# Kernel optimization log

Measured on AMD Instinct MI355X. Metric: run time of the kernel, lower is better.

## Reference

```python
import jax, jax.numpy as jnp
import numpy as np

B = 8192
MOTION_DIM = 512
COMMAND_DIM = 64
HIDDEN = 1024
E = 8  # num_experts
NUM_LAYERS = 6


def _dense(key, shape, fan_in):
    return jax.random.normal(key, shape, dtype=jnp.float32) * (1.0 / np.sqrt(fan_in))


def setup_inputs() -> dict:
    key = jax.random.key(0)
    ks = jax.random.split(key, 32)
    in_dim = MOTION_DIM + COMMAND_DIM  # 576
    inp = {
        "motion": jax.random.normal(ks[0], (B, MOTION_DIM), dtype=jnp.float32),
        "command": jax.random.normal(ks[1], (B, COMMAND_DIM), dtype=jnp.float32),
        # gating network: in -> H -> H -> E, ELU, softmax
        "g_w1": _dense(ks[2], (in_dim, HIDDEN), in_dim),
        "g_b1": jnp.zeros((HIDDEN,), jnp.float32),
        "g_w2": _dense(ks[3], (HIDDEN, HIDDEN), HIDDEN),
        "g_b2": jnp.zeros((HIDDEN,), jnp.float32),
        "g_w3": _dense(ks[4], (HIDDEN, E), HIDDEN),
        "g_b3": jnp.zeros((E,), jnp.float32),
        # MoE layers: dims [in->H, H->H, H->H, H->H, H->H?, ...] per CMG layout
        "w0": _dense(ks[5], (E, in_dim, HIDDEN), in_dim),
        "b0": jnp.zeros((E, HIDDEN), jnp.float32),
        "w1": _dense(ks[6], (E, HIDDEN, HIDDEN), HIDDEN),
        "b1": jnp.zeros((E, HIDDEN), jnp.float32),
        "w2": _dense(ks[7], (E, HIDDEN, HIDDEN), HIDDEN),
        "b2": jnp.zeros((E, HIDDEN), jnp.float32),
        "w3": _dense(ks[8], (E, HIDDEN, HIDDEN), HIDDEN),
        "b3": jnp.zeros((E, HIDDEN), jnp.float32),
        "w4": _dense(ks[9], (E, HIDDEN, HIDDEN), HIDDEN),
        "b4": jnp.zeros((E, HIDDEN), jnp.float32),
        "w5": _dense(ks[10], (E, HIDDEN, MOTION_DIM), HIDDEN),
        "b5": jnp.zeros((E, MOTION_DIM), jnp.float32),
    }
    return inp


def _moe_layer(x, coeffs, W, b):
    # x: [B, din], coeffs: [B, E], W: [E, din, dout], b: [E, dout]
    # y[b] = sum_e coeffs[b,e] * (x[b] @ W[e] + b[e])
    y = jnp.einsum("be,bi,eio->bo", coeffs, x, W)
    y = y + jnp.einsum("be,eo->bo", coeffs, b)
    return y


def _cmg_forward(motion, command,
                 g_w1, g_b1, g_w2, g_b2, g_w3, g_b3,
                 w0, b0, w1, b1, w2, b2, w3, b3, w4, b4, w5, b5):
    x = jnp.concatenate([motion, command], axis=-1)  # [B, in_dim]
    # gating network
    g = jax.nn.elu(x @ g_w1 + g_b1)
    g = jax.nn.elu(g @ g_w2 + g_b2)
    coeffs = jax.nn.softmax(g @ g_w3 + g_b3, axis=-1)  # [B, E]
    # stacked MoE layers with ELU between all but last
    Ws = [w0, w1, w2, w3, w4, w5]
    bs = [b0, b1, b2, b3, b4, b5]
    for i in range(NUM_LAYERS):
        x = _moe_layer(x, coeffs, Ws[i], bs[i])
        if i < NUM_LAYERS - 1:
            x = jax.nn.elu(x)
    return x  # [B, MOTION_DIM]


def reference(motion, command,
              g_w1, g_b1, g_w2, g_b2, g_w3, g_b3,
              w0, b0, w1, b1, w2, b2, w3, b3, w4, b4, w5, b5):
    return _cmg_forward(motion, command,
                        g_w1, g_b1, g_w2, g_b2, g_w3, g_b3,
                        w0, b0, w1, b1, w2, b2, w3, b3, w4, b4, w5, b5)
```

## Files before the change

kernel.cpp:

```cpp
#include <hip/hip_runtime.h>
#include <hip/hip_bf16.h>

typedef __attribute__((ext_vector_type(8))) short bf16x8;
typedef __attribute__((ext_vector_type(4))) float f32x4;

__device__ __forceinline__ float bf2f(unsigned short u) {
    union { unsigned int i; float f; } v; v.i = ((unsigned int)u) << 16; return v.f;
}
__device__ __forceinline__ unsigned short f2bf(float f) {
    union { float f; unsigned int i; } v; v.f = f;
    unsigned int x = v.i;
    return (unsigned short)((x + 0x7FFFu + ((x >> 16) & 1u)) >> 16);
}

__device__ __forceinline__ void gload_lds16(const unsigned short* g, unsigned short* l) {
    __builtin_amdgcn_global_load_lds(
        (const __attribute__((address_space(1))) unsigned int*)g,
        (__attribute__((address_space(3))) unsigned int*)l,
        16, 0, 0);
}

#define VM4  asm volatile("s_waitcnt vmcnt(4)" ::: "memory")
#define VM0  asm volatile("s_waitcnt vmcnt(0)" ::: "memory")
#define LG0  asm volatile("s_waitcnt lgkmcnt(0)" ::: "memory")
#define SB0  __builtin_amdgcn_sched_barrier(0)

__global__ void concat_cvt(const float* __restrict__ motion,
                           const float* __restrict__ command,
                           unsigned short* __restrict__ out) {
    int id = blockIdx.x * 256 + threadIdx.x;
    int b = id / 144, q = id % 144;
    float4 v;
    if (q < 128) v = *(const float4*)(motion + (size_t)b * 512 + q * 4);
    else         v = *(const float4*)(command + (size_t)b * 64 + (q - 128) * 4);
    ushort4 o;
    o.x = f2bf(v.x); o.y = f2bf(v.y); o.z = f2bf(v.z); o.w = f2bf(v.w);
    *(ushort4*)(out + (size_t)b * 576 + q * 4) = o;
}

__global__ void transpose_cvt(const float* __restrict__ in,
                              unsigned short* __restrict__ out,
                              int K, int N, int tpe) {
    __shared__ unsigned short tile[64][72];
    int e = blockIdx.x / tpe, r = blockIdx.x % tpe;
    in  += (size_t)e * K * N;
    out += (size_t)e * N * K;
    int nbn = N / 64;
    int k0 = (r / nbn) * 64;
    int n0 = (r % nbn) * 64;
    int t = threadIdx.x;
    int tx = t & 63, ty = t >> 6;
    #pragma unroll
    for (int rr = 0; rr < 16; ++rr) {
        int kr = ty + rr * 4;
        tile[kr][tx] = f2bf(in[(size_t)(k0 + kr) * N + n0 + tx]);
    }
    __syncthreads();
    int txh = t & 31, tyh = t >> 5;
    #pragma unroll
    for (int rr = 0; rr < 8; ++rr) {
        int nr = tyh + rr * 8;
        unsigned int vlo = tile[2 * txh][nr];
        unsigned int vhi = tile[2 * txh + 1][nr];
        unsigned int* o32 = (unsigned int*)(out + (size_t)(n0 + nr) * K + k0);
        o32[txh] = vlo | (vhi << 16);
    }
}

__global__ __launch_bounds__(256) void gating_kernel(
    const unsigned short* __restrict__ g2,
    const float* __restrict__ w3, const float* __restrict__ b3,
    float* __restrict__ coeffs) {
    __shared__ float w3s[8][1024];
    int t = threadIdx.x;
    for (int i = t; i < 1024; i += 256) {
        #pragma unroll
        for (int e = 0; e < 8; ++e) w3s[e][i] = w3[(size_t)i * 8 + e];
    }
    __syncthreads();
    int lane = t & 63, wv = t >> 6;
    int row = blockIdx.x * 4 + wv;
    const unsigned short* xr = g2 + (size_t)row * 1024;
    float acc[8];
    #pragma unroll
    for (int e = 0; e < 8; ++e) acc[e] = 0.f;
    for (int it = 0; it < 16; ++it) {
        float xv = bf2f(xr[lane + it * 64]);
        #pragma unroll
        for (int e = 0; e < 8; ++e) acc[e] += xv * w3s[e][lane + it * 64];
    }
    #pragma unroll
    for (int e = 0; e < 8; ++e) {
        float v = acc[e];
        #pragma unroll
        for (int off = 32; off; off >>= 1) v += __shfl_xor(v, off);
        acc[e] = v + b3[e];
    }
    float mx = acc[0];
    #pragma unroll
    for (int e = 1; e < 8; ++e) mx = fmaxf(mx, acc[e]);
    float s = 0.f;
    #pragma unroll
    for (int e = 0; e < 8; ++e) { acc[e] = __expf(acc[e] - mx); s += acc[e]; }
    float inv = 1.f / s;
    if (lane < 8) coeffs[(size_t)row * 8 + lane] = acc[lane] * inv;
}

template<bool DO_ELU>
__global__ __launch_bounds__(256, 4)
void gemm_bf16(const unsigned short* __restrict__ A,
               const unsigned short* __restrict__ BT,
               const float* __restrict__ bias,
               unsigned short* __restrict__ Out,
               int N, int ld, int kpart) {
    __shared__ unsigned short As[128 * 64];
    __shared__ unsigned short Bs[128 * 64];
    int ntn = N >> 7;
    int nwg = gridDim.x;
    int bid = blockIdx.x;
    { int cpx = nwg >> 3; bid = (bid & 7) * cpx + (bid >> 3); }
    int tm = bid / ntn, tn = bid - tm * ntn;
    int row0 = tm << 7, col0 = tn << 7;
    int t = threadIdx.x;
    int lane = t & 63;
    int wid = t >> 6;
    int wr = wid >> 1, wc = wid & 1;
    const unsigned short* Ab = A + (size_t)(row0 + wid * 32 + (lane >> 3)) * ld + (lane & 7) * 8;
    const unsigned short* Bb = BT + (size_t)(col0 + wid * 32 + (lane >> 3)) * ld + (lane & 7) * 8;
    unsigned short* Asd = &As[wid * 32 * 64];
    unsigned short* Bsd = &Bs[wid * 32 * 64];
    f32x4 acc[4][4];
    #pragma unroll
    for (int i = 0; i < 4; ++i)
        #pragma unroll
        for (int j = 0; j < 4; ++j) acc[i][j] = (f32x4){0.f, 0.f, 0.f, 0.f};
    int nkt = kpart >> 6;
    for (int kt = 0; kt < nkt; ++kt) {
        size_t ko = (size_t)kt << 6;
        #pragma unroll
        for (int q = 0; q < 4; ++q) {
            gload_lds16(Ab + (size_t)(q * 8) * ld + ko, Asd + q * 8 * 64);
            gload_lds16(Bb + (size_t)(q * 8) * ld + ko, Bsd + q * 8 * 64);
        }
        __syncthreads();
        #pragma unroll
        for (int kk = 0; kk < 2; ++kk) {
            bf16x8 af[4], bfr[4];
            #pragma unroll
            for (int m = 0; m < 4; ++m)
                af[m] = *(const bf16x8*)(&As[(wr * 64 + m * 16 + (lane & 15)) * 64 + kk * 32 + (lane >> 4) * 8]);
            #pragma unroll
            for (int n = 0; n < 4; ++n)
                bfr[n] = *(const bf16x8*)(&Bs[(wc * 64 + n * 16 + (lane & 15)) * 64 + kk * 32 + (lane >> 4) * 8]);
            #pragma unroll
            for (int m = 0; m < 4; ++m)
                #pragma unroll
                for (int n = 0; n < 4; ++n)
                    acc[m][n] = __builtin_amdgcn_mfma_f32_16x16x32_bf16(af[m], bfr[n], acc[m][n], 0, 0, 0);
        }
        __syncthreads();
    }
    #pragma unroll
    for (int m = 0; m < 4; ++m) {
        int rbase = row0 + wr * 64 + m * 16 + ((lane >> 4) << 2);
        #pragma unroll
        for (int n = 0; n < 4; ++n) {
            int cg = col0 + wc * 64 + n * 16 + (lane & 15);
            float bv = bias[cg];
            #pragma unroll
            for (int r2 = 0; r2 < 4; ++r2) {
                float v = acc[m][n][r2] + bv;
                if (DO_ELU) v = v > 0.f ? v : (__expf(v) - 1.f);
                Out[(size_t)(rbase + r2) * N + cg] = f2bf(v);
            }
        }
    }
}

template<bool DO_ELU, bool OUT_F32>
__global__ __launch_bounds__(512, 1)
void gemm_fused(const unsigned short* __restrict__ A,
                const unsigned short* __restrict__ BT,
                const float* __restrict__ coeffs,
                const float* __restrict__ bias,
                void* __restrict__ Out,
                int K, int dout) {
    __shared__ unsigned short lds[65536];

    int ntn = dout >> 5;
    int nwg = gridDim.x;
    int bid = blockIdx.x;
    { int cpx = nwg >> 3; bid = (bid & 7) * cpx + (bid >> 3); }
    int tm = bid / ntn, tn = bid - tm * ntn;
    int row0 = tm << 8;
    int c0 = tn << 5;
    int nkt = K >> 5;

    int t = threadIdx.x;
    int lane = t & 63, wid = t >> 6;
    int wm = wid >> 2, wn = wid & 3;
    int q = lane >> 4;

    int aoff[8], boff[4];
    #pragma unroll
    for (int m = 0; m < 8; ++m) {
        int row = wm * 128 + m * 16 + (lane & 15);
        aoff[m] = row * 32 + ((q ^ ((row >> 1) & 3)) << 3);
    }
    #pragma unroll
    for (int n = 0; n < 4; ++n) {
        int row = wn * 64 + n * 16 + (lane & 15);
        boff[n] = 8192 + row * 32 + ((q ^ ((row >> 1) & 3)) << 3);
    }

    int srow = t >> 2;
    int scol = ((t & 3) ^ ((t >> 3) & 3)) * 8;
    const unsigned short* Asrc = A + (size_t)(row0 + srow) * K + scol;
    int br0 = (srow >> 5) * dout + c0 + (srow & 31);
    int br1 = ((srow + 128) >> 5) * dout + c0 + (srow & 31);
    const unsigned short* Bsrc0 = BT + (size_t)br0 * K + scol;
    const unsigned short* Bsrc1 = BT + (size_t)br1 * K + scol;
    int wdst = wid * 512;

    f32x4 acc[8][4];
    #pragma unroll
    for (int m = 0; m < 8; ++m)
        #pragma unroll
        for (int n = 0; n < 4; ++n) acc[m][n] = (f32x4){0.f, 0.f, 0.f, 0.f};

    #pragma unroll
    for (int S = 0; S < 2; ++S) {
        gload_lds16(Asrc + S * 32,                   &lds[S * 16384 + wdst]);
        gload_lds16(Asrc + (size_t)128 * K + S * 32, &lds[S * 16384 + 4096 + wdst]);
        gload_lds16(Bsrc0 + S * 32,                  &lds[S * 16384 + 8192 + wdst]);
        gload_lds16(Bsrc1 + S * 32,                  &lds[S * 16384 + 12288 + wdst]);
    }
    VM4; SB0;
    __builtin_amdgcn_s_barrier();

    for (int s = 0; s < nkt; ++s) {
        int sb = (s & 3) << 14;
        bool st = (s + 2) < nkt;
        int rb2 = ((s + 2) & 3) << 14;
        int ko2 = (s + 2) * 32;

        if (st) {
            gload_lds16(Asrc + ko2,                   &lds[rb2 + wdst]);
            gload_lds16(Asrc + (size_t)128 * K + ko2, &lds[rb2 + 4096 + wdst]);
            gload_lds16(Bsrc0 + ko2,                  &lds[rb2 + 8192 + wdst]);
            gload_lds16(Bsrc1 + ko2,                  &lds[rb2 + 12288 + wdst]);
        }
        SB0;
        if (s + 1 < nkt) {
            if (st) { VM4; } else { VM0; }
        }
        SB0;
        __builtin_amdgcn_s_barrier();
        SB0;

        bf16x8 bfrg[4], afr[8];
        #pragma unroll
        for (int n = 0; n < 4; ++n)
            bfrg[n] = *(const bf16x8*)(&lds[sb + boff[n]]);
        #pragma unroll
        for (int m = 0; m < 8; ++m)
            afr[m] = *(const bf16x8*)(&lds[sb + aoff[m]]);
        __builtin_amdgcn_s_setprio(1);
        #pragma unroll
        for (int m = 0; m < 8; ++m)
            #pragma unroll
            for (int n = 0; n < 4; ++n)
                acc[m][n] = __builtin_amdgcn_mfma_f32_16x16x32_bf16(bfrg[n], afr[m], acc[m][n], 0, 0, 0);
        __builtin_amdgcn_s_setprio(0);
        SB0;
    }

    float* plds = (float*)lds;
    __syncthreads();
    {
        int e0 = 2 * wn, e1 = e0 + 1;
        f32x4 b0h[2], b1h[2];
        #pragma unroll
        for (int h = 0; h < 2; ++h) {
            float4 u0 = *(const float4*)(bias + e0 * dout + c0 + h * 16 + q * 4);
            float4 u1 = *(const float4*)(bias + e1 * dout + c0 + h * 16 + q * 4);
            b0h[h] = (f32x4){u0.x, u0.y, u0.z, u0.w};
            b1h[h] = (f32x4){u1.x, u1.y, u1.z, u1.w};
        }
        float* preg = plds + (wid << 12);
        #pragma unroll
        for (int m = 0; m < 8; ++m) {
            int grow = row0 + wm * 128 + m * 16 + (lane & 15);
            float c8 = coeffs[(size_t)grow * 8 + e0];
            float c9 = coeffs[(size_t)grow * 8 + e1];
            #pragma unroll
            for (int h = 0; h < 2; ++h) {
                f32x4 z0 = acc[m][h];
                f32x4 z1 = acc[m][h + 2];
                f32x4 p;
                #pragma unroll
                for (int r = 0; r < 4; ++r)
                    p[r] = c8 * (z0[r] + b0h[h][r]) + c9 * (z1[r] + b1h[h][r]);
                int row = m * 16 + (lane & 15);
                int slot = (h * 4 + q) ^ (row & 7);
                *(f32x4*)(preg + row * 32 + (slot << 2)) = p;
            }
        }
    }
    __syncthreads();

    {
        int r2 = t >> 1;
        int ch = t & 1;
        int wmr = r2 >> 7;
        int rr = r2 & 127;
        int sw = rr & 7;
        size_t obase = (size_t)(row0 + r2) * dout + c0 + ch * 16;
        #pragma unroll
        for (int sl = 0; sl < 4; ++sl) {
            int L = ch * 4 + sl;
            int phys = L ^ sw;
            f32x4 sum = (f32x4){0.f, 0.f, 0.f, 0.f};
            #pragma unroll
            for (int w2 = 0; w2 < 4; ++w2) {
                const f32x4 v = *(const f32x4*)(plds + (((wmr << 2) + w2) << 12) + rr * 32 + (phys << 2));
                sum[0] += v[0]; sum[1] += v[1]; sum[2] += v[2]; sum[3] += v[3];
            }
            if (DO_ELU) {
                #pragma unroll
                for (int r = 0; r < 4; ++r)
                    sum[r] = sum[r] > 0.f ? sum[r] : (__expf(sum[r]) - 1.f);
            }
            if (OUT_F32) {
                float4 o = {sum[0], sum[1], sum[2], sum[3]};
                *(float4*)((float*)Out + obase + sl * 4) = o;
            } else {
                ushort4 o;
                o.x = f2bf(sum[0]); o.y = f2bf(sum[1]);
                o.z = f2bf(sum[2]); o.w = f2bf(sum[3]);
                *(ushort4*)((unsigned short*)Out + obase + sl * 4) = o;
            }
        }
    }
}

extern "C" void kernel_launch(void* const* d_in, const int* in_sizes, int n_in,
                              void* d_out, int out_size, void* d_ws, size_t ws_size,
                              hipStream_t stream) {
    const float* motion  = (const float*)d_in[0];
    const float* command = (const float*)d_in[1];
    const float* g_w1 = (const float*)d_in[2];
    const float* g_b1 = (const float*)d_in[3];
    const float* g_w2 = (const float*)d_in[4];
    const float* g_b2 = (const float*)d_in[5];
    const float* g_w3 = (const float*)d_in[6];
    const float* g_b3 = (const float*)d_in[7];
    const float* w[6]  = {(const float*)d_in[8],  (const float*)d_in[10],
                          (const float*)d_in[12], (const float*)d_in[14],
                          (const float*)d_in[16], (const float*)d_in[18]};
    const float* bb[6] = {(const float*)d_in[9],  (const float*)d_in[11],
                          (const float*)d_in[13], (const float*)d_in[15],
                          (const float*)d_in[17], (const float*)d_in[19]};

    char* ws = (char*)d_ws;
    unsigned short* xc0  = (unsigned short*)ws;
    unsigned short* actA = (unsigned short*)(ws + 9437184);
    unsigned short* actB = (unsigned short*)(ws + 26214400);
    float* coeffs        = (float*)(ws + 42991616);
    unsigned short* wT   = (unsigned short*)(ws + 43253760);

    concat_cvt<<<4608, 256, 0, stream>>>(motion, command, xc0);

    transpose_cvt<<<144, 256, 0, stream>>>(g_w1, wT, 576, 1024, 144);
    gemm_bf16<true><<<512, 256, 0, stream>>>(xc0, wT, g_b1, actA, 1024, 576, 576);
    transpose_cvt<<<256, 256, 0, stream>>>(g_w2, wT, 1024, 1024, 256);
    gemm_bf16<true><<<512, 256, 0, stream>>>(actA, wT, g_b2, actB, 1024, 1024, 1024);
    gating_kernel<<<2048, 256, 0, stream>>>(actB, g_w3, g_b3, coeffs);

    transpose_cvt<<<1152, 256, 0, stream>>>(w[0], wT, 576, 1024, 144);
    gemm_fused<true, false><<<1024, 512, 0, stream>>>(
        xc0, wT, coeffs, bb[0], actA, 576, 1024);

    unsigned short* bufs[2] = {actA, actB};
    for (int l = 1; l <= 4; ++l) {
        unsigned short* in  = bufs[(l + 1) & 1];
        unsigned short* out = bufs[l & 1];
        transpose_cvt<<<2048, 256, 0, stream>>>(w[l], wT, 1024, 1024, 256);
        gemm_fused<true, false><<<1024, 512, 0, stream>>>(
            in, wT, coeffs, bb[l], out, 1024, 1024);
    }

    transpose_cvt<<<1024, 256, 0, stream>>>(w[5], wT, 1024, 512, 128);
    gemm_fused<false, true><<<512, 512, 0, stream>>>(
        actA, wT, coeffs, bb[5], d_out, 1024, 512);
}
```

Before: 791.6 us.

## Process two K-tiles per barrier and remap workgroups to 4x4 tile groups

The fused MoE GEMM main loop now consumes two 32-wide K-tiles per iteration. It issues prefetches for the next two tiles after a single full vmcnt wait and barrier, where before each tile had its own partial wait and barrier. Workgroup-to-tile mapping changes from a strided XCD swizzle to 4x4 groups of row and column tiles per XCD, to improve L2 reuse of A and B. The cost is a coarser wait: it drains all outstanding loads each step. The mapping and loop also assume 32 row tiles, column-tile counts divisible by 4, and an even number of K-tiles.

```diff
diff --git a/kernel.cpp b/kernel.cpp
--- a/kernel.cpp
+++ b/kernel.cpp
@@ -20,10 +20,9 @@
         16, 0, 0);
 }
 
-#define VM4  asm volatile("s_waitcnt vmcnt(4)" ::: "memory")
 #define VM0  asm volatile("s_waitcnt vmcnt(0)" ::: "memory")
-#define LG0  asm volatile("s_waitcnt lgkmcnt(0)" ::: "memory")
 #define SB0  __builtin_amdgcn_sched_barrier(0)
+#define BAR  __builtin_amdgcn_s_barrier()
 
 __global__ void concat_cvt(const float* __restrict__ motion,
                            const float* __restrict__ command,
@@ -187,11 +186,12 @@
                 int K, int dout) {
     __shared__ unsigned short lds[65536];
 
-    int ntn = dout >> 5;
-    int nwg = gridDim.x;
     int bid = blockIdx.x;
-    { int cpx = nwg >> 3; bid = (bid & 7) * cpx + (bid >> 3); }
-    int tm = bid / ntn, tn = bid - tm * ntn;
+    int x = bid & 7;
+    int i = bid >> 3;
+    int within = i & 15;
+    int tm = x * 4 + (within & 3);
+    int tn = (i >> 4) * 4 + (within >> 2);
     int row0 = tm << 8;
     int c0 = tn << 5;
     int nkt = K >> 5;
@@ -200,16 +200,17 @@
     int lane = t & 63, wid = t >> 6;
     int wm = wid >> 2, wn = wid & 3;
     int q = lane >> 4;
+    int l15 = lane & 15;
 
     int aoff[8], boff[4];
     #pragma unroll
     for (int m = 0; m < 8; ++m) {
-        int row = wm * 128 + m * 16 + (lane & 15);
+        int row = wm * 128 + m * 16 + l15;
         aoff[m] = row * 32 + ((q ^ ((row >> 1) & 3)) << 3);
     }
     #pragma unroll
     for (int n = 0; n < 4; ++n) {
-        int row = wn * 64 + n * 16 + (lane & 15);
+        int row = wn * 64 + n * 16 + l15;
         boff[n] = 8192 + row * 32 + ((q ^ ((row >> 1) & 3)) << 3);
     }
 
@@ -235,43 +236,62 @@
         gload_lds16(Bsrc0 + S * 32,                  &lds[S * 16384 + 8192 + wdst]);
         gload_lds16(Bsrc1 + S * 32,                  &lds[S * 16384 + 12288 + wdst]);
     }
-    VM4; SB0;
-    __builtin_amdgcn_s_barrier();
-
-    for (int s = 0; s < nkt; ++s) {
-        int sb = (s & 3) << 14;
+
+    for (int s = 0; s < nkt; s += 2) {
+        int sbA = (s & 3) << 14;
+        int sbB = ((s + 1) & 3) << 14;
         bool st = (s + 2) < nkt;
-        int rb2 = ((s + 2) & 3) << 14;
-        int ko2 = (s + 2) * 32;
-
+
+        VM0; SB0;
+        BAR;
         if (st) {
-            gload_lds16(Asrc + ko2,                   &lds[rb2 + wdst]);
-            gload_lds16(Asrc + (size_t)128 * K + ko2, &lds[rb2 + 4096 + wdst]);
-            gload_lds16(Bsrc0 + ko2,                  &lds[rb2 + 8192 + wdst]);
-            gload_lds16(Bsrc1 + ko2,                  &lds[rb2 + 12288 + wdst]);
+            int rbA = ((s + 2) & 3) << 14;
+            int rbB = ((s + 3) & 3) << 14;
+            int koA = (s + 2) << 5;
+            int koB = (s + 3) << 5;
+            gload_lds16(Asrc + koA,                   &lds[rbA + wdst]);
+            gload_lds16(Asrc + (size_t)128 * K + koA, &lds[rbA + 4096 + wdst]);
+            gload_lds16(Bsrc0 + koA,                  &lds[rbA + 8192 + wdst]);
+            gload_lds16(Bsrc1 + koA,                  &lds[rbA + 12288 + wdst]);
+            gload_lds16(Asrc + koB,                   &lds[rbB + wdst]);
+            gload_lds16(Asrc + (size_t)128 * K + koB, &lds[rbB + 4096 + wdst]);
+            gload_lds16(Bsrc0 + koB,                  &lds[rbB + 8192 + wdst]);
+            gload_lds16(Bsrc1 + koB,                  &lds[rbB + 12288 + wdst]);
         }
         SB0;
-        if (s + 1 < nkt) {
-            if (st) { VM4; } else { VM0; }
-        }
-        SB0;
-        __builtin_amdgcn_s_barrier();
-        SB0;
-
-        bf16x8 bfrg[4], afr[8];
-        #pragma unroll
-        for (int n = 0; n < 4; ++n)
-            bfrg[n] = *(const bf16x8*)(&lds[sb + boff[n]]);
-        #pragma unroll
-        for (int m = 0; m < 8; ++m)
-            afr[m] = *(const bf16x8*)(&lds[sb + aoff[m]]);
-        __builtin_amdgcn_s_setprio(1);
-        #pragma unroll
-        for (int m = 0; m < 8; ++m)
+
+        {
+            bf16x8 bfrg[4], afr[8];
             #pragma unroll
             for (int n = 0; n < 4; ++n)
-                acc[m][n] = __builtin_amdgcn_mfma_f32_16x16x32_bf16(bfrg[n], afr[m], acc[m][n], 0, 0, 0);
-        __builtin_amdgcn_s_setprio(0);
+                bfrg[n] = *(const bf16x8*)(&lds[sbA + boff[n]]);
+            #pragma unroll
+            for (int m = 0; m < 8; ++m)
+                afr[m] = *(const bf16x8*)(&lds[sbA + aoff[m]]);
+            __builtin_amdgcn_s_setprio(1);
+            #pragma unroll
+            for (int m = 0; m < 8; ++m)
+                #pragma unroll
+                for (int n = 0; n < 4; ++n)
+                    acc[m][n] = __builtin_amdgcn_mfma_f32_16x16x32_bf16(bfrg[n], afr[m], acc[m][n], 0, 0, 0);
+            __builtin_amdgcn_s_setprio(0);
+        }
+        {
+            bf16x8 bfrg[4], afr[8];
+            #pragma unroll
+            for (int n = 0; n < 4; ++n)
+                bfrg[n] = *(const bf16x8*)(&lds[sbB + boff[n]]);
+            #pragma unroll
+            for (int m = 0; m < 8; ++m)
+                afr[m] = *(const bf16x8*)(&lds[sbB + aoff[m]]);
+            __builtin_amdgcn_s_setprio(1);
+            #pragma unroll
+            for (int m = 0; m < 8; ++m)
+                #pragma unroll
+                for (int n = 0; n < 4; ++n)
+                    acc[m][n] = __builtin_amdgcn_mfma_f32_16x16x32_bf16(bfrg[n], afr[m], acc[m][n], 0, 0, 0);
+            __builtin_amdgcn_s_setprio(0);
+        }
         SB0;
     }
 
@@ -290,7 +310,7 @@
         float* preg = plds + (wid << 12);
         #pragma unroll
         for (int m = 0; m < 8; ++m) {
-            int grow = row0 + wm * 128 + m * 16 + (lane & 15);
+            int grow = row0 + wm * 128 + m * 16 + l15;
             float c8 = coeffs[(size_t)grow * 8 + e0];
             float c9 = coeffs[(size_t)grow * 8 + e1];
             #pragma unroll
@@ -301,7 +321,7 @@
                 #pragma unroll
                 for (int r = 0; r < 4; ++r)
                     p[r] = c8 * (z0[r] + b0h[h][r]) + c9 * (z1[r] + b1h[h][r]);
-                int row = m * 16 + (lane & 15);
+                int row = m * 16 + l15;
                 int slot = (h * 4 + q) ^ (row & 7);
                 *(f32x4*)(preg + row * 32 + (slot << 2)) = p;
             }
```

New measurement: 736.0 us. 7.0% less time.
